# Kernel optimization log

Measured on AMD Instinct MI355X. Metric: run time of the kernel, lower is better.

## Reference

```python
import jax, jax.numpy as jnp
import numpy as np

N, E, F, H = 100000, 1600000, 128, 128


def setup_inputs() -> dict:
    key = jax.random.key(0)
    ks = jax.random.split(key, 32)
    def w(i, shape):
        fan_in = shape[0]
        return jax.random.normal(ks[i], shape, dtype=jnp.float32) / np.sqrt(fan_in)
    inp = {
        'x': jax.random.normal(ks[0], (N, F), dtype=jnp.float32),
        't': jax.random.randint(ks[1], (N,), 0, 2, dtype=jnp.int32),
        'z': jax.random.normal(ks[2], (N, H), dtype=jnp.float32),
        'edge_index': jax.random.randint(ks[3], (2, E), 0, N, dtype=jnp.int32),
        # GCNConv weights (PyG: out = scatter(norm * (xW)) + b)
        'W_o': w(4, (F, H)), 'b_o': jnp.zeros((H,), jnp.float32),
        'W_t': w(5, (F, H)), 'b_t': jnp.zeros((H,), jnp.float32),
        # masked attention: Linear(2H, 1)
        'a_w': w(6, (2 * H, 1)), 'a_b': jnp.zeros((1,), jnp.float32),
        # encoder_final: Linear(2H, H)
        'W_enc': w(7, (2 * H, H)), 'b_enc': jnp.zeros((H,), jnp.float32),
        # predictor heads (3 linears each)
        'p1_W1': w(8, (H, H)), 'p1_b1': jnp.zeros((H,), jnp.float32),
        'p1_W2': w(9, (H, H)), 'p1_b2': jnp.zeros((H,), jnp.float32),
        'p1_W3': w(10, (H, 1)), 'p1_b3': jnp.zeros((1,), jnp.float32),
        'p0_W1': w(11, (H, H)), 'p0_b1': jnp.zeros((H,), jnp.float32),
        'p0_W2': w(12, (H, H)), 'p0_b2': jnp.zeros((H,), jnp.float32),
        'p0_W3': w(13, (H, 1)), 'p0_b3': jnp.zeros((1,), jnp.float32),
        # discriminator head
        'd_W1': w(14, (H, H)), 'd_b1': jnp.zeros((H,), jnp.float32),
        'd_W2': w(15, (H, H)), 'd_b2': jnp.zeros((H,), jnp.float32),
        'd_W3': w(16, (H, 1)), 'd_b3': jnp.zeros((1,), jnp.float32),
    }
    return inp


def _mlp3(x, W1, b1, W2, b2, W3, b3):
    h = jax.nn.leaky_relu(x @ W1 + b1, 0.2)
    h = jax.nn.leaky_relu(h @ W2 + b2, 0.2)
    return h @ W3 + b3


def _gcn(x, W, b, src, dst, norm, n):
    xw = x @ W                                   # [N,H]
    agg = jax.ops.segment_sum(xw[src] * norm[:, None], dst, num_segments=n)
    return agg + b


def reference(x, t, z, edge_index, W_o, b_o, W_t, b_t, a_w, a_b, W_enc, b_enc,
              p1_W1, p1_b1, p1_W2, p1_b2, p1_W3, p1_b3,
              p0_W1, p0_b1, p0_W2, p0_b2, p0_W3, p0_b3,
              d_W1, d_b1, d_W2, d_b2, d_W3, d_b3):
    n = x.shape[0]
    src, dst = edge_index[0], edge_index[1]
    # --- GCN with self-loops and symmetric normalization ---
    loop = jnp.arange(n, dtype=src.dtype)
    src2 = jnp.concatenate([src, loop])
    dst2 = jnp.concatenate([dst, loop])
    deg = jax.ops.segment_sum(jnp.ones_like(dst2, jnp.float32), dst2, num_segments=n)
    dinv = jax.lax.rsqrt(deg)                    # deg >= 1 (self loops)
    norm = dinv[src2] * dinv[dst2]               # [E+N]
    r_o = jax.nn.relu(_gcn(x, W_o, b_o, src2, dst2, norm, n))
    r_t = jax.nn.relu(_gcn(x, W_t, b_t, src2, dst2, norm, n))
    cat = jnp.concatenate([r_o, r_t], axis=-1)   # [N,2H]
    # --- masked attention over edges: only treated sources attend ---
    e = (cat @ a_w + a_b)[:, 0]                  # [N]
    logits = jax.nn.leaky_relu(e[src] + e[dst], 0.2)   # [E]
    mask = (t[src] > 0).astype(jnp.float32)
    m = jax.ops.segment_max(logits, dst, num_segments=n)
    m = jnp.where(jnp.isfinite(m), m, 0.0)
    w = jnp.exp(logits - m[dst]) * mask
    denom = jax.ops.segment_sum(w, dst, num_segments=n) + 1e-16
    alpha = w / denom[dst]                       # [E]
    h = jax.ops.segment_sum(r_t[src] * alpha[:, None], dst, num_segments=n)  # [N,H]
    # --- heads ---
    z_enc = jnp.concatenate([r_o, h], axis=-1) @ W_enc + b_enc   # [N,H]
    pred_1 = _mlp3(z_enc, p1_W1, p1_b1, p1_W2, p1_b2, p1_W3, p1_b3)[:, 0]
    pred_0 = _mlp3(z_enc, p0_W1, p0_b1, p0_W2, p0_b2, p0_W3, p0_b3)[:, 0]
    pred = jnp.where(t > 0, pred_1, pred_0)[:, None]             # [N,1]
    pred_t = jax.nn.sigmoid(_mlp3(r_t, d_W1, d_b1, d_W2, d_b2, d_W3, d_b3))  # [N,1]
    return pred_t, pred, z_enc
```

## Files before the change

### kernel.cpp

```cpp
#include <hip/hip_runtime.h>
#include <hip/hip_bf16.h>
#include <math.h>


using bf16x8 = __attribute__((ext_vector_type(8))) short;
using s16x8  = __attribute__((ext_vector_type(8))) short;
using f32x4  = __attribute__((ext_vector_type(4))) float;

static __device__ __forceinline__ float lrelu02(float x) { return x > 0.f ? x : 0.2f * x; }

static __device__ __forceinline__ unsigned short f2bf(float f) {
    unsigned u = __float_as_uint(f);
    unsigned r = u + 0x7FFF + ((u >> 16) & 1);
    return (unsigned short)(r >> 16);
}
static __device__ __forceinline__ float bf2f(unsigned short h) {
    return __uint_as_float(((unsigned)h) << 16);
}
static __device__ __forceinline__ float bflo(unsigned u) { return __uint_as_float(u << 16); }
static __device__ __forceinline__ float bfhi(unsigned u) { return __uint_as_float(u & 0xFFFF0000u); }


__global__ void k_zero_i32(int* __restrict__ p, int n) {
    int i = blockIdx.x * blockDim.x + threadIdx.x;
    int stride = gridDim.x * blockDim.x;
    for (; i < n; i += stride) p[i] = 0;
}

__global__ void k_copy_i32(const int* __restrict__ a, int* __restrict__ b, int n) {
    int i = blockIdx.x * blockDim.x + threadIdx.x;
    if (i < n) b[i] = a[i];
}

__global__ __launch_bounds__(256) void k_bhist(const int* __restrict__ src,
                                               const int* __restrict__ dst,
                                               const int* __restrict__ t,
                                               int* __restrict__ bhist,
                                               int* __restrict__ bhist_m,
                                               int e, int shift) {
    __shared__ int h[256], hm[256];
    h[threadIdx.x] = 0; hm[threadIdx.x] = 0;
    __syncthreads();
    int i = blockIdx.x * blockDim.x + threadIdx.x;
    int stride = gridDim.x * blockDim.x;
    for (; i < e; i += stride) {
        int b = dst[i] >> shift;
        atomicAdd(&h[b], 1);
        if (t[src[i]] > 0) atomicAdd(&hm[b], 1);
    }
    __syncthreads();
    if (h[threadIdx.x]) atomicAdd(&bhist[threadIdx.x], h[threadIdx.x]);
    if (hm[threadIdx.x]) atomicAdd(&bhist_m[threadIdx.x], hm[threadIdx.x]);
}

__global__ __launch_bounds__(256) void k_scanb(const int* __restrict__ bsum,
                                               int* __restrict__ boff, int nb) {
    __shared__ int s[256];
    int t = threadIdx.x;
    int v = (t < nb) ? bsum[t] : 0;
    s[t] = v;
    __syncthreads();
    for (int off = 1; off < 256; off <<= 1) {
        int u = (t >= off) ? s[t - off] : 0;
        __syncthreads();
        s[t] += u;
        __syncthreads();
    }
    if (t < nb) boff[t] = s[t] - v;
    if (t == nb - 1) boff[nb] = s[t];
}

__global__ __launch_bounds__(256) void k_fillB(const int* __restrict__ src,
                                               const int* __restrict__ dst,
                                               const int* __restrict__ t,
                                               int* __restrict__ bcur,
                                               int* __restrict__ ebuf,
                                               int e, int shift) {
    __shared__ int h[256];
    const int EPT = 16;
    int blk_base = blockIdx.x * 256 * EPT;
    h[threadIdx.x] = 0;
    __syncthreads();
    int pk[EPT], bk[EPT];
#pragma unroll
    for (int j = 0; j < EPT; ++j) {
        int i = blk_base + threadIdx.x + j * 256;
        if (i < e) {
            int s = src[i], d = dst[i];
            int b = d >> shift;
            bk[j] = b;
            int tb = (t[s] > 0) ? 1 : 0;
            pk[j] = s | ((d - (b << shift)) << 20) | (tb << 29);
            atomicAdd(&h[b], 1);
        } else bk[j] = -1;
    }
    __syncthreads();
    int cnt = h[threadIdx.x];
    int base = 0;
    if (cnt > 0) base = atomicAdd(&bcur[threadIdx.x], cnt);
    __syncthreads();
    h[threadIdx.x] = base;
    __syncthreads();
#pragma unroll
    for (int j = 0; j < EPT; ++j) {
        if (bk[j] >= 0) {
            int pos = atomicAdd(&h[bk[j]], 1);
            ebuf[pos] = pk[j];
        }
    }
}

__global__ __launch_bounds__(256) void k_sortC(const int* __restrict__ ebuf,
                                               const int* __restrict__ bbase,
                                               const int* __restrict__ bbase_m,
                                               int* __restrict__ indptr,
                                               int* __restrict__ indptr_m,
                                               float* __restrict__ dinv,
                                               int* __restrict__ out_all,
                                               int* __restrict__ out_m,
                                               int n, int shift, int NB) {
    __shared__ int cnt[512], cnt_m[512];
    __shared__ int cur[512], cur_m[512];
    __shared__ int tmp[256];
    int tid = threadIdx.x;
    int b = blockIdx.x;
    int lo = bbase[b], hi = bbase[b + 1];
    int lom = bbase_m[b];
    int dbase = b << shift;
    for (int j = tid; j < 512; j += 256) { cnt[j] = 0; cnt_m[j] = 0; }
    __syncthreads();
    for (int i = lo + tid; i < hi; i += 256) {
        int pk = ebuf[i];
        int dlo = (pk >> 20) & 511;
        atomicAdd(&cnt[dlo], 1);
        if (pk >> 29) atomicAdd(&cnt_m[dlo], 1);
    }
    __syncthreads();
    int c0 = cnt[2 * tid], c1 = cnt[2 * tid + 1];
    int ps = c0 + c1;
    tmp[tid] = ps;
    __syncthreads();
    for (int off = 1; off < 256; off <<= 1) {
        int u = (tid >= off) ? tmp[tid - off] : 0;
        __syncthreads();
        tmp[tid] += u;
        __syncthreads();
    }
    int pre = tmp[tid] - ps;
    cur[2 * tid] = pre;
    cur[2 * tid + 1] = pre + c0;
    __syncthreads();
    int m0 = cnt_m[2 * tid], m1 = cnt_m[2 * tid + 1];
    int psm = m0 + m1;
    tmp[tid] = psm;
    __syncthreads();
    for (int off = 1; off < 256; off <<= 1) {
        int u = (tid >= off) ? tmp[tid - off] : 0;
        __syncthreads();
        tmp[tid] += u;
        __syncthreads();
    }
    int prem = tmp[tid] - psm;
    cur_m[2 * tid] = prem;
    cur_m[2 * tid + 1] = prem + m0;
    __syncthreads();
    int nd = n - dbase; if (nd > 512) nd = 512;
    for (int j = tid; j < nd; j += 256) {
        indptr[dbase + j] = lo + cur[j];
        indptr_m[dbase + j] = lom + cur_m[j];
        dinv[dbase + j] = rsqrtf((float)cnt[j] + 1.0f);
    }
    if (b == 0 && tid == 0) {
        indptr[n] = bbase[NB];
        indptr_m[n] = bbase_m[NB];
    }
    __syncthreads();
    for (int i = lo + tid; i < hi; i += 256) {
        int pk = ebuf[i];
        int s = pk & 0xFFFFF;
        int dlo = (pk >> 20) & 511;
        int pos = lo + atomicAdd(&cur[dlo], 1);
        out_all[pos] = s;
        if (pk >> 29) {
            int pm = lom + atomicAdd(&cur_m[dlo], 1);
            out_m[pm] = s;
        }
    }
}


__global__ void k_cvt_pre(const float* __restrict__ x, const float* __restrict__ dinv,
                          unsigned short* __restrict__ xp, int total4) {
    int i = blockIdx.x * blockDim.x + threadIdx.x;
    int stride = gridDim.x * blockDim.x;
    for (; i < total4; i += stride) {
        float dv = dinv[i >> 5];
        float4 v = ((const float4*)x)[i];
        ushort4 o;
        o.x = f2bf(v.x * dv); o.y = f2bf(v.y * dv);
        o.z = f2bf(v.z * dv); o.w = f2bf(v.w * dv);
        ((ushort4*)xp)[i] = o;
    }
}

__global__ void k_wt(const float* __restrict__ W, unsigned short* __restrict__ Wt,
                     int K, int Nc) {
    int i = blockIdx.x * blockDim.x + threadIdx.x;
    if (i >= K * Nc) return;
    int k = i / Nc, j = i % Nc;
    Wt[(size_t)j * K + k] = f2bf(W[i]);
}

__global__ void k_wcat_t(const float* __restrict__ Wo, const float* __restrict__ Wt_in,
                         unsigned short* __restrict__ Wt) {
    int i = blockIdx.x * blockDim.x + threadIdx.x;
    if (i >= 256 * 128) return;
    int j = i >> 7, k = i & 127;
    float v = (j < 128) ? Wo[(k << 7) + j] : Wt_in[(k << 7) + j - 128];
    Wt[i] = f2bf(v);
}

__global__ __launch_bounds__(256) void k_aggx(const unsigned short* __restrict__ xp,
                                              const int* __restrict__ indptr,
                                              const int* __restrict__ srcs,
                                              const float* __restrict__ dinv,
                                              unsigned short* __restrict__ aggx, int n) {
    int wv = threadIdx.x >> 6, lane = threadIdx.x & 63;
    int v = blockIdx.x * 4 + wv;
    if (v >= n) return;
    const unsigned* xp2 = (const unsigned*)xp;
    int beg = indptr[v], end = indptr[v + 1];
    unsigned sv = xp2[(size_t)v * 64 + lane];
    float a0 = bflo(sv), a1 = bfhi(sv);
    int i = beg;
    for (; i + 8 <= end; i += 8) {
        int s0 = srcs[i], s1 = srcs[i + 1], s2 = srcs[i + 2], s3 = srcs[i + 3];
        int s4 = srcs[i + 4], s5 = srcs[i + 5], s6 = srcs[i + 6], s7 = srcs[i + 7];
        unsigned u0 = xp2[(size_t)s0 * 64 + lane];
        unsigned u1 = xp2[(size_t)s1 * 64 + lane];
        unsigned u2 = xp2[(size_t)s2 * 64 + lane];
        unsigned u3 = xp2[(size_t)s3 * 64 + lane];
        unsigned u4 = xp2[(size_t)s4 * 64 + lane];
        unsigned u5 = xp2[(size_t)s5 * 64 + lane];
        unsigned u6 = xp2[(size_t)s6 * 64 + lane];
        unsigned u7 = xp2[(size_t)s7 * 64 + lane];
        a0 += bflo(u0) + bflo(u1) + bflo(u2) + bflo(u3)
            + bflo(u4) + bflo(u5) + bflo(u6) + bflo(u7);
        a1 += bfhi(u0) + bfhi(u1) + bfhi(u2) + bfhi(u3)
            + bfhi(u4) + bfhi(u5) + bfhi(u6) + bfhi(u7);
    }
    for (; i + 4 <= end; i += 4) {
        int s0 = srcs[i], s1 = srcs[i + 1], s2 = srcs[i + 2], s3 = srcs[i + 3];
        unsigned u0 = xp2[(size_t)s0 * 64 + lane];
        unsigned u1 = xp2[(size_t)s1 * 64 + lane];
        unsigned u2 = xp2[(size_t)s2 * 64 + lane];
        unsigned u3 = xp2[(size_t)s3 * 64 + lane];
        a0 += bflo(u0) + bflo(u1) + bflo(u2) + bflo(u3);
        a1 += bfhi(u0) + bfhi(u1) + bfhi(u2) + bfhi(u3);
    }
    for (; i < end; ++i) {
        unsigned u = xp2[(size_t)srcs[i] * 64 + lane];
        a0 += bflo(u); a1 += bfhi(u);
    }
    float dv = dinv[v];
    a0 *= dv; a1 *= dv;
    unsigned o = (unsigned)f2bf(a0) | ((unsigned)f2bf(a1) << 16);
    ((unsigned*)aggx)[(size_t)v * 64 + lane] = o;
}

__global__ __launch_bounds__(256) void k_gcn(const unsigned short* __restrict__ aggx,
                                             const unsigned short* __restrict__ Wcat,
                                             const float* __restrict__ b_o,
                                             const float* __restrict__ b_t,
                                             const float* __restrict__ a_w,
                                             const float* __restrict__ a_b,
                                             unsigned short* __restrict__ cat2,
                                             unsigned short* __restrict__ rt,
                                             float* __restrict__ e, int M) {
    __shared__ short ct[64][264];
    int wave = threadIdx.x >> 6, lane = threadIdx.x & 63;
    int row_base = blockIdx.x * 64 + wave * 16;
    int rA = row_base + (lane & 15);
    if (rA >= M) rA = M - 1;
    int koff = (lane >> 4) << 3;
    int colL = lane & 15;

    bf16x8 a[4];
#pragma unroll
    for (int ks = 0; ks < 4; ++ks)
        a[ks] = *(const bf16x8*)((const short*)aggx + (size_t)rA * 128 + (ks << 5) + koff);

    f32x4 acc[16];
#pragma unroll
    for (int cf = 0; cf < 16; ++cf) acc[cf] = (f32x4){0.f, 0.f, 0.f, 0.f};
#pragma unroll
    for (int ks = 0; ks < 4; ++ks)
#pragma unroll
        for (int cf = 0; cf < 16; ++cf) {
            bf16x8 b = *(const bf16x8*)((const short*)Wcat + (size_t)((cf << 4) + colL) * 128 + (ks << 5) + koff);
            acc[cf] = __builtin_amdgcn_mfma_f32_16x16x32_bf16(a[ks], b, acc[cf], 0, 0, 0);
        }

    float ep0 = 0.f, ep1 = 0.f, ep2 = 0.f, ep3 = 0.f;
    int rl0 = wave * 16 + ((lane >> 4) << 2);
#pragma unroll
    for (int cf = 0; cf < 16; ++cf) {
        int col = (cf << 4) + colL;
        float bv = (col < 128) ? b_o[col] : b_t[col - 128];
        float aw = a_w[col];
#pragma unroll
        for (int j = 0; j < 4; ++j) {
            float v = fmaxf(acc[cf][j] + bv, 0.f);
            if (j == 0) ep0 += v * aw;
            else if (j == 1) ep1 += v * aw;
            else if (j == 2) ep2 += v * aw;
            else ep3 += v * aw;
            ct[rl0 + j][col] = (short)f2bf(v);
        }
    }
#pragma unroll
    for (int mk = 1; mk < 16; mk <<= 1) {
        ep0 += __shfl_xor(ep0, mk); ep1 += __shfl_xor(ep1, mk);
        ep2 += __shfl_xor(ep2, mk); ep3 += __shfl_xor(ep3, mk);
    }
    if (colL == 0) {
        float ab = a_b[0];
        int r0 = row_base + ((lane >> 4) << 2);
        if (r0 + 0 < M) e[r0 + 0] = ep0 + ab;
        if (r0 + 1 < M) e[r0 + 1] = ep1 + ab;
        if (r0 + 2 < M) e[r0 + 2] = ep2 + ab;
        if (r0 + 3 < M) e[r0 + 3] = ep3 + ab;
    }
    __syncthreads();
    int base64 = blockIdx.x * 64;
    short* cp = (short*)cat2 + (size_t)base64 * 256;
    for (int j = threadIdx.x; j < 1024; j += 256) {
        int row = j >> 4;
        if (base64 + row < M)
            *(s16x8*)(cp + (size_t)row * 256 + ((j & 15) << 3)) =
                *(const s16x8*)&ct[row][(j & 15) << 3];
    }
    short* rp = (short*)rt + (size_t)base64 * 128;
    for (int j = threadIdx.x; j < 1024; j += 256) {
        int row = j >> 4;
        if (base64 + row < M)
            *(s16x8*)(rp + (size_t)row * 128 + ((j & 15) << 3)) =
                *(const s16x8*)&ct[row][128 + ((j & 15) << 3)];
    }
}

__global__ __launch_bounds__(256) void k_attn(const unsigned short* __restrict__ rt,
                                              const int* __restrict__ indptr_m,
                                              const int* __restrict__ srcs_m,
                                              const float* __restrict__ e,
                                              unsigned short* __restrict__ cat2, int n) {
    int wv = threadIdx.x >> 6, lane = threadIdx.x & 63;
    int v = blockIdx.x * 4 + wv;
    if (v >= n) return;
    float ev = e[v];
    int bm = indptr_m[v], em = indptr_m[v + 1];
    float m = -INFINITY;
    for (int i = bm + lane; i < em; i += 64)
        m = fmaxf(m, lrelu02(ev + e[srcs_m[i]]));
    for (int off = 32; off; off >>= 1) m = fmaxf(m, __shfl_xor(m, off));
    if (bm == em) m = 0.f;
    float h0 = 0.f, h1 = 0.f, wsum = 0.f;
    const unsigned* rt2 = (const unsigned*)rt;
    int i = bm;
    for (; i + 8 <= em; i += 8) {
        int s0 = srcs_m[i], s1 = srcs_m[i + 1], s2 = srcs_m[i + 2], s3 = srcs_m[i + 3];
        int s4 = srcs_m[i + 4], s5 = srcs_m[i + 5], s6 = srcs_m[i + 6], s7 = srcs_m[i + 7];
        float w0 = __expf(lrelu02(ev + e[s0]) - m);
        float w1 = __expf(lrelu02(ev + e[s1]) - m);
        float w2 = __expf(lrelu02(ev + e[s2]) - m);
        float w3 = __expf(lrelu02(ev + e[s3]) - m);
        float w4 = __expf(lrelu02(ev + e[s4]) - m);
        float w5 = __expf(lrelu02(ev + e[s5]) - m);
        float w6 = __expf(lrelu02(ev + e[s6]) - m);
        float w7 = __expf(lrelu02(ev + e[s7]) - m);
        unsigned u0 = rt2[(size_t)s0 * 64 + lane];
        unsigned u1 = rt2[(size_t)s1 * 64 + lane];
        unsigned u2 = rt2[(size_t)s2 * 64 + lane];
        unsigned u3 = rt2[(size_t)s3 * 64 + lane];
        unsigned u4 = rt2[(size_t)s4 * 64 + lane];
        unsigned u5 = rt2[(size_t)s5 * 64 + lane];
        unsigned u6 = rt2[(size_t)s6 * 64 + lane];
        unsigned u7 = rt2[(size_t)s7 * 64 + lane];
        wsum += w0 + w1 + w2 + w3 + w4 + w5 + w6 + w7;
        h0 += w0 * bflo(u0) + w1 * bflo(u1) + w2 * bflo(u2) + w3 * bflo(u3)
            + w4 * bflo(u4) + w5 * bflo(u5) + w6 * bflo(u6) + w7 * bflo(u7);
        h1 += w0 * bfhi(u0) + w1 * bfhi(u1) + w2 * bfhi(u2) + w3 * bfhi(u3)
            + w4 * bfhi(u4) + w5 * bfhi(u5) + w6 * bfhi(u6) + w7 * bfhi(u7);
    }
    for (; i < em; ++i) {
        int s = srcs_m[i];
        float w = __expf(lrelu02(ev + e[s]) - m);
        unsigned u = rt2[(size_t)s * 64 + lane];
        wsum += w;
        h0 += w * bflo(u);
        h1 += w * bfhi(u);
    }
    float inv = 1.f / (wsum + 1e-16f);
    unsigned o = (unsigned)f2bf(h0 * inv) | ((unsigned)f2bf(h1 * inv) << 16);
    ((unsigned*)(cat2 + (size_t)v * 256 + 128))[lane] = o;
}

__global__ __launch_bounds__(256) void k_tail(
    const unsigned short* __restrict__ cat2, const unsigned short* __restrict__ rt_bf,
    const unsigned short* __restrict__ Wenc, const float* __restrict__ b_enc,
    const unsigned short* __restrict__ W11, const float* __restrict__ b11,
    const unsigned short* __restrict__ W12, const float* __restrict__ b12,
    const float* __restrict__ W13, const float* __restrict__ b13,
    const unsigned short* __restrict__ W01, const float* __restrict__ b01,
    const unsigned short* __restrict__ W02, const float* __restrict__ b02,
    const float* __restrict__ W03, const float* __restrict__ b03,
    const unsigned short* __restrict__ Wd1, const float* __restrict__ bd1,
    const unsigned short* __restrict__ Wd2, const float* __restrict__ bd2,
    const float* __restrict__ Wd3, const float* __restrict__ bd3,
    const int* __restrict__ t, float* __restrict__ zenc,
    float* __restrict__ out, int M) {
    __shared__ __align__(16) char pool[128 * 136 * 2 + 64 * 136 * 2];
    short* Wa = (short*)pool;
    short* hb = (short*)(pool + 128 * 136 * 2);
    float* zt = (float*)pool;

    int wave = threadIdx.x >> 6, lane = threadIdx.x & 63;
    int row_base = blockIdx.x * 64 + wave * 16;
    int rA = row_base + (lane & 15);
    if (rA >= M) rA = M - 1;
    int koff = (lane >> 4) << 3;
    int colL = lane & 15;
    int base64 = blockIdx.x * 64;

    bf16x8 ra[4];
#pragma unroll
    for (int ks = 0; ks < 4; ++ks)
        ra[ks] = *(const bf16x8*)((const short*)rt_bf + (size_t)rA * 128 + (ks << 5) + koff);

    {
        const short* Ap = (const short*)cat2 + (size_t)rA * 256 + koff;
        const short* Bp = (const short*)Wenc + (size_t)colL * 256 + koff;
        f32x4 acc[8];
#pragma unroll
        for (int cf = 0; cf < 8; ++cf) acc[cf] = (f32x4){0.f, 0.f, 0.f, 0.f};
#pragma unroll
        for (int ks = 0; ks < 8; ++ks) {
            bf16x8 a = *(const bf16x8*)(Ap + (ks << 5));
#pragma unroll
            for (int cf = 0; cf < 8; ++cf) {
                bf16x8 b = *(const bf16x8*)(Bp + (size_t)(cf << 4) * 256 + (ks << 5));
                acc[cf] = __builtin_amdgcn_mfma_f32_16x16x32_bf16(a, b, acc[cf], 0, 0, 0);
            }
        }
        int rl0 = wave * 16 + ((lane >> 4) << 2);
#pragma unroll
        for (int cf = 0; cf < 8; ++cf) {
            int col = (cf << 4) + colL;
            float bv = b_enc[col];
#pragma unroll
            for (int j = 0; j < 4; ++j)
                zt[(rl0 + j) * 132 + col] = acc[cf][j] + bv;
        }
    }
    __syncthreads();
    {
        float* zp = zenc + (size_t)base64 * 128;
        for (int j = threadIdx.x; j < 2048; j += 256) {
            int row = j >> 5;
            if (base64 + row < M)
                *(float4*)(zp + (size_t)j * 4) = *(const float4*)&zt[row * 132 + ((j & 31) << 2)];
        }
    }
    bf16x8 za[4];
    {
        int rAl = wave * 16 + (lane & 15);
#pragma unroll
        for (int ks = 0; ks < 4; ++ks) {
            float4 v0 = *(const float4*)&zt[rAl * 132 + (ks << 5) + koff];
            float4 v1 = *(const float4*)&zt[rAl * 132 + (ks << 5) + koff + 4];
            za[ks][0] = (short)f2bf(v0.x); za[ks][1] = (short)f2bf(v0.y);
            za[ks][2] = (short)f2bf(v0.z); za[ks][3] = (short)f2bf(v0.w);
            za[ks][4] = (short)f2bf(v1.x); za[ks][5] = (short)f2bf(v1.y);
            za[ks][6] = (short)f2bf(v1.z); za[ks][7] = (short)f2bf(v1.w);
        }
    }

    float sp1[4], sp0[4], sdd[4];

    auto stage = [&](const unsigned short* W) {
        for (int i = threadIdx.x; i < 2048; i += 256) {
            int r = i >> 4, c = (i & 15) << 3;
            bf16x8 v = *(const bf16x8*)((const short*)W + (r << 7) + c);
            *(bf16x8*)(Wa + r * 136 + c) = v;
        }
    };

    auto run_head = [&](const bf16x8* A0,
                        const unsigned short* W1, const float* b1,
                        const unsigned short* W2, const float* b2,
                        const float* W3, const float* b3, float* sout) {
        __syncthreads();
        stage(W1);
        __syncthreads();
        f32x4 acc[8];
#pragma unroll
        for (int cf = 0; cf < 8; ++cf) acc[cf] = (f32x4){0.f, 0.f, 0.f, 0.f};
#pragma unroll
        for (int ks = 0; ks < 4; ++ks)
#pragma unroll
            for (int cf = 0; cf < 8; ++cf) {
                bf16x8 b = *(const bf16x8*)(Wa + ((cf << 4) + colL) * 136 + (ks << 5) + koff);
                acc[cf] = __builtin_amdgcn_mfma_f32_16x16x32_bf16(A0[ks], b, acc[cf], 0, 0, 0);
            }
        short* hw = hb + wave * 2176;
#pragma unroll
        for (int cf = 0; cf < 8; ++cf) {
            int col = (cf << 4) + colL;
            float bv = b1[col];
#pragma unroll
            for (int j = 0; j < 4; ++j)
                hw[(((lane >> 4) << 2) + j) * 136 + col] = (short)f2bf(lrelu02(acc[cf][j] + bv));
        }
        __syncthreads();
        stage(W2);
        __syncthreads();
        bf16x8 h1f[4];
#pragma unroll
        for (int ks = 0; ks < 4; ++ks)
            h1f[ks] = *(const bf16x8*)(hw + colL * 136 + (ks << 5) + koff);
#pragma unroll
        for (int cf = 0; cf < 8; ++cf) acc[cf] = (f32x4){0.f, 0.f, 0.f, 0.f};
#pragma unroll
        for (int ks = 0; ks < 4; ++ks)
#pragma unroll
            for (int cf = 0; cf < 8; ++cf) {
                bf16x8 b = *(const bf16x8*)(Wa + ((cf << 4) + colL) * 136 + (ks << 5) + koff);
                acc[cf] = __builtin_amdgcn_mfma_f32_16x16x32_bf16(h1f[ks], b, acc[cf], 0, 0, 0);
            }
        float s0 = 0.f, s1 = 0.f, s2 = 0.f, s3 = 0.f;
#pragma unroll
        for (int cf = 0; cf < 8; ++cf) {
            int col = (cf << 4) + colL;
            float w3 = W3[col], bv = b2[col];
            s0 += lrelu02(acc[cf][0] + bv) * w3;
            s1 += lrelu02(acc[cf][1] + bv) * w3;
            s2 += lrelu02(acc[cf][2] + bv) * w3;
            s3 += lrelu02(acc[cf][3] + bv) * w3;
        }
#pragma unroll
        for (int mk = 1; mk < 16; mk <<= 1) {
            s0 += __shfl_xor(s0, mk); s1 += __shfl_xor(s1, mk);
            s2 += __shfl_xor(s2, mk); s3 += __shfl_xor(s3, mk);
        }
        float bb = b3[0];
        sout[0] = s0 + bb; sout[1] = s1 + bb; sout[2] = s2 + bb; sout[3] = s3 + bb;
    };

    run_head(za, W11, b11, W12, b12, W13, b13, sp1);
    run_head(za, W01, b01, W02, b02, W03, b03, sp0);
    run_head(ra, Wd1, bd1, Wd2, bd2, Wd3, bd3, sdd);

    if (colL == 0) {
#pragma unroll
        for (int j = 0; j < 4; ++j) {
            int row = row_base + ((lane >> 4) << 2) + j;
            if (row < M) {
                out[row] = 1.f / (1.f + __expf(-sdd[j]));
                out[M + row] = (t[row] > 0) ? sp1[j] : sp0[j];
            }
        }
    }
}


extern "C" void kernel_launch(void* const* d_in, const int* in_sizes, int n_in,
                              void* d_out, int out_size, void* d_ws, size_t ws_size,
                              hipStream_t stream) {
    const float* x     = (const float*)d_in[0];
    const int*   t     = (const int*)d_in[1];
    const int*   ei    = (const int*)d_in[3];
    const float* W_o   = (const float*)d_in[4];
    const float* b_o   = (const float*)d_in[5];
    const float* W_t   = (const float*)d_in[6];
    const float* b_t   = (const float*)d_in[7];
    const float* a_w   = (const float*)d_in[8];
    const float* a_b   = (const float*)d_in[9];
    const float* W_enc = (const float*)d_in[10];
    const float* b_enc = (const float*)d_in[11];
    const float* p1_W1 = (const float*)d_in[12]; const float* p1_b1 = (const float*)d_in[13];
    const float* p1_W2 = (const float*)d_in[14]; const float* p1_b2 = (const float*)d_in[15];
    const float* p1_W3 = (const float*)d_in[16]; const float* p1_b3 = (const float*)d_in[17];
    const float* p0_W1 = (const float*)d_in[18]; const float* p0_b1 = (const float*)d_in[19];
    const float* p0_W2 = (const float*)d_in[20]; const float* p0_b2 = (const float*)d_in[21];
    const float* p0_W3 = (const float*)d_in[22]; const float* p0_b3 = (const float*)d_in[23];
    const float* d_W1  = (const float*)d_in[24]; const float* d_b1  = (const float*)d_in[25];
    const float* d_W2  = (const float*)d_in[26]; const float* d_b2  = (const float*)d_in[27];
    const float* d_W3  = (const float*)d_in[28]; const float* d_b3  = (const float*)d_in[29];

    const int n = in_sizes[1];
    const int E = in_sizes[3] / 2;
    const int* src = ei;
    const int* dst = ei + E;

    float* out  = (float*)d_out;
    float* zenc = out + 2 * (size_t)n;

    const int shift = 9;
    const int NB = (n + (1 << shift) - 1) >> shift;

    char* base = (char*)d_ws;
    size_t o = 0;
    auto alloc = [&](size_t bytes) { char* p = base + o; o += (bytes + 255) & ~(size_t)255; return p; };
    unsigned short* xp_bf   = (unsigned short*)alloc((size_t)n * 128 * 2);
    unsigned short* aggx_bf = (unsigned short*)alloc((size_t)n * 128 * 2);
    unsigned short* cat2_bf = (unsigned short*)alloc((size_t)n * 256 * 2);
    unsigned short* rt_bf   = (unsigned short*)alloc((size_t)n * 128 * 2);
    float* dinv = (float*)alloc((size_t)n * 4);
    float* evec = (float*)alloc((size_t)n * 4);
    unsigned short* Wcat_t = (unsigned short*)alloc(256 * 128 * 2);
    unsigned short* Wenc_t = (unsigned short*)alloc(128 * 256 * 2);
    unsigned short* Wp1a_t = (unsigned short*)alloc(128 * 128 * 2);
    unsigned short* Wp1b_t = (unsigned short*)alloc(128 * 128 * 2);
    unsigned short* Wp0a_t = (unsigned short*)alloc(128 * 128 * 2);
    unsigned short* Wp0b_t = (unsigned short*)alloc(128 * 128 * 2);
    unsigned short* Wda_t  = (unsigned short*)alloc(128 * 128 * 2);
    unsigned short* Wdb_t  = (unsigned short*)alloc(128 * 128 * 2);
    int* indptr     = (int*)alloc(((size_t)n + 1) * 4);
    int* indptr_m   = (int*)alloc(((size_t)n + 1) * 4);
    int* bhist      = (int*)alloc(257 * 4);
    int* bhist_m    = (int*)alloc(257 * 4);
    int* bbase      = (int*)alloc(257 * 4);
    int* bbase_m    = (int*)alloc(257 * 4);
    int* bcur       = (int*)alloc(257 * 4);
    int* src_sorted = (int*)alloc((size_t)E * 4);
    int* src_mask   = (int*)alloc((size_t)E * 4);
    int* ebuf       = (int*)alloc((size_t)E * 4);

    const int mt = (n + 63) / 64;

    k_zero_i32<<<1, 256, 0, stream>>>(bhist, 257);
    k_zero_i32<<<1, 256, 0, stream>>>(bhist_m, 257);
    k_bhist<<<1024, 256, 0, stream>>>(src, dst, t, bhist, bhist_m, E, shift);
    k_scanb<<<1, 256, 0, stream>>>(bhist, bbase, NB);
    k_scanb<<<1, 256, 0, stream>>>(bhist_m, bbase_m, NB);
    k_copy_i32<<<1, 256, 0, stream>>>(bbase, bcur, NB);
    k_fillB<<<(E + 4095) / 4096, 256, 0, stream>>>(src, dst, t, bcur, ebuf, E, shift);
    k_sortC<<<NB, 256, 0, stream>>>(ebuf, bbase, bbase_m, indptr, indptr_m, dinv,
                                    src_sorted, src_mask, n, shift, NB);

    k_cvt_pre<<<2048, 256, 0, stream>>>(x, dinv, xp_bf, n * 32);
    k_wcat_t<<<128, 256, 0, stream>>>(W_o, W_t, Wcat_t);
    k_wt<<<128, 256, 0, stream>>>(W_enc, Wenc_t, 256, 128);
    k_wt<<<64, 256, 0, stream>>>(p1_W1, Wp1a_t, 128, 128);
    k_wt<<<64, 256, 0, stream>>>(p1_W2, Wp1b_t, 128, 128);
    k_wt<<<64, 256, 0, stream>>>(p0_W1, Wp0a_t, 128, 128);
    k_wt<<<64, 256, 0, stream>>>(p0_W2, Wp0b_t, 128, 128);
    k_wt<<<64, 256, 0, stream>>>(d_W1, Wda_t, 128, 128);
    k_wt<<<64, 256, 0, stream>>>(d_W2, Wdb_t, 128, 128);

    k_aggx<<<(n + 3) / 4, 256, 0, stream>>>(xp_bf, indptr, src_sorted, dinv, aggx_bf, n);

    k_gcn<<<mt, 256, 0, stream>>>(aggx_bf, Wcat_t, b_o, b_t, a_w, a_b,
                                  cat2_bf, rt_bf, evec, n);

    k_attn<<<(n + 3) / 4, 256, 0, stream>>>(rt_bf, indptr_m, src_mask, evec, cat2_bf, n);

    k_tail<<<mt, 256, 0, stream>>>(cat2_bf, rt_bf, Wenc_t, b_enc,
                                   Wp1a_t, p1_b1, Wp1b_t, p1_b2, p1_W3, p1_b3,
                                   Wp0a_t, p0_b1, Wp0b_t, p0_b2, p0_W3, p0_b3,
                                   Wda_t, d_b1, Wdb_t, d_b2, d_W3, d_b3,
                                   t, zenc, out, n);
}
```

Measured before the change: 443.6 us.

## Process 128 rows per tail block and merge small setup kernels

```diff
diff --git a/kernel.cpp b/kernel.cpp
--- a/kernel.cpp
+++ b/kernel.cpp
@@ -25,11 +25,6 @@
     int i = blockIdx.x * blockDim.x + threadIdx.x;
     int stride = gridDim.x * blockDim.x;
     for (; i < n; i += stride) p[i] = 0;
-}
-
-__global__ void k_copy_i32(const int* __restrict__ a, int* __restrict__ b, int n) {
-    int i = blockIdx.x * blockDim.x + threadIdx.x;
-    if (i < n) b[i] = a[i];
 }
 
 __global__ __launch_bounds__(256) void k_bhist(const int* __restrict__ src,
@@ -53,11 +48,14 @@
     if (hm[threadIdx.x]) atomicAdd(&bhist_m[threadIdx.x], hm[threadIdx.x]);
 }
 
-__global__ __launch_bounds__(256) void k_scanb(const int* __restrict__ bsum,
-                                               int* __restrict__ boff, int nb) {
+__global__ __launch_bounds__(256) void k_scan2(const int* __restrict__ bhist,
+                                               const int* __restrict__ bhist_m,
+                                               int* __restrict__ bbase,
+                                               int* __restrict__ bbase_m,
+                                               int* __restrict__ bcur, int nb) {
     __shared__ int s[256];
     int t = threadIdx.x;
-    int v = (t < nb) ? bsum[t] : 0;
+    int v = (t < nb) ? bhist[t] : 0;
     s[t] = v;
     __syncthreads();
     for (int off = 1; off < 256; off <<= 1) {
@@ -66,8 +64,20 @@
         s[t] += u;
         __syncthreads();
     }
-    if (t < nb) boff[t] = s[t] - v;
-    if (t == nb - 1) boff[nb] = s[t];
+    if (t < nb) { bbase[t] = s[t] - v; bcur[t] = s[t] - v; }
+    if (t == nb - 1) bbase[nb] = s[t];
+    __syncthreads();
+    int v2 = (t < nb) ? bhist_m[t] : 0;
+    s[t] = v2;
+    __syncthreads();
+    for (int off = 1; off < 256; off <<= 1) {
+        int u = (t >= off) ? s[t - off] : 0;
+        __syncthreads();
+        s[t] += u;
+        __syncthreads();
+    }
+    if (t < nb) bbase_m[t] = s[t] - v2;
+    if (t == nb - 1) bbase_m[nb] = s[t];
 }
 
 __global__ __launch_bounds__(256) void k_fillB(const int* __restrict__ src,
@@ -203,21 +213,39 @@
     }
 }
 
-__global__ void k_wt(const float* __restrict__ W, unsigned short* __restrict__ Wt,
-                     int K, int Nc) {
-    int i = blockIdx.x * blockDim.x + threadIdx.x;
-    if (i >= K * Nc) return;
-    int k = i / Nc, j = i % Nc;
-    Wt[(size_t)j * K + k] = f2bf(W[i]);
-}
-
-__global__ void k_wcat_t(const float* __restrict__ Wo, const float* __restrict__ Wt_in,
-                         unsigned short* __restrict__ Wt) {
-    int i = blockIdx.x * blockDim.x + threadIdx.x;
-    if (i >= 256 * 128) return;
-    int j = i >> 7, k = i & 127;
-    float v = (j < 128) ? Wo[(k << 7) + j] : Wt_in[(k << 7) + j - 128];
-    Wt[i] = f2bf(v);
+__global__ void k_wprep(const float* __restrict__ Wo, const float* __restrict__ Wti,
+                        const float* __restrict__ Wenc,
+                        const float* __restrict__ p1W1, const float* __restrict__ p1W2,
+                        const float* __restrict__ p0W1, const float* __restrict__ p0W2,
+                        const float* __restrict__ dW1, const float* __restrict__ dW2,
+                        unsigned short* __restrict__ Wcat_t,
+                        unsigned short* __restrict__ Wenc_t,
+                        unsigned short* __restrict__ o1, unsigned short* __restrict__ o2,
+                        unsigned short* __restrict__ o3, unsigned short* __restrict__ o4,
+                        unsigned short* __restrict__ o5, unsigned short* __restrict__ o6) {
+    int idx = blockIdx.x * 256 + threadIdx.x;
+    if (idx < 32768) {
+        int j = idx >> 7, k = idx & 127;
+        float v = (j < 128) ? Wo[(k << 7) + j] : Wti[(k << 7) + j - 128];
+        Wcat_t[idx] = f2bf(v);
+    } else if (idx < 65536) {
+        int i = idx - 32768;
+        Wenc_t[(size_t)(i & 127) * 256 + (i >> 7)] = f2bf(Wenc[i]);
+    } else {
+        int i2 = idx - 65536;
+        int h = i2 >> 14;
+        int i = i2 & 16383;
+        const float* W; unsigned short* O;
+        switch (h) {
+            case 0: W = p1W1; O = o1; break;
+            case 1: W = p1W2; O = o2; break;
+            case 2: W = p0W1; O = o3; break;
+            case 3: W = p0W2; O = o4; break;
+            case 4: W = dW1;  O = o5; break;
+            default: W = dW2; O = o6; break;
+        }
+        O[(i & 127) * 128 + (i >> 7)] = f2bf(W[i]);
+    }
 }
 
 __global__ __launch_bounds__(256) void k_aggx(const unsigned short* __restrict__ xp,
@@ -419,26 +447,29 @@
     const float* __restrict__ Wd3, const float* __restrict__ bd3,
     const int* __restrict__ t, float* __restrict__ zenc,
     float* __restrict__ out, int M) {
-    __shared__ __align__(16) char pool[128 * 136 * 2 + 64 * 136 * 2];
+    const int WS = 132;
+    const int ZS = 133;
+    __shared__ __align__(16) char pool[64 * 133 * 4 + 64 * 132 * 2];
     short* Wa = (short*)pool;
-    short* hb = (short*)(pool + 128 * 136 * 2);
     float* zt = (float*)pool;
+    short* hb = (short*)(pool + 64 * 133 * 4);
 
     int wave = threadIdx.x >> 6, lane = threadIdx.x & 63;
-    int row_base = blockIdx.x * 64 + wave * 16;
-    int rA = row_base + (lane & 15);
-    if (rA >= M) rA = M - 1;
+    int colL = lane & 15;
     int koff = (lane >> 4) << 3;
-    int colL = lane & 15;
-    int base64 = blockIdx.x * 64;
-
-    bf16x8 ra[4];
-#pragma unroll
-    for (int ks = 0; ks < 4; ++ks)
-        ra[ks] = *(const bf16x8*)((const short*)rt_bf + (size_t)rA * 128 + (ks << 5) + koff);
-
-    {
-        const short* Ap = (const short*)cat2 + (size_t)rA * 256 + koff;
+    int base128 = blockIdx.x * 128;
+
+    int rAc[2];
+#pragma unroll
+    for (int c = 0; c < 2; ++c) {
+        int rA = base128 + c * 64 + wave * 16 + colL;
+        rAc[c] = (rA >= M) ? M - 1 : rA;
+    }
+
+    bf16x8 za[2][4];
+#pragma unroll
+    for (int c = 0; c < 2; ++c) {
+        const short* Ap = (const short*)cat2 + (size_t)rAc[c] * 256 + koff;
         const short* Bp = (const short*)Wenc + (size_t)colL * 256 + koff;
         f32x4 acc[8];
 #pragma unroll
@@ -459,116 +490,133 @@
             float bv = b_enc[col];
 #pragma unroll
             for (int j = 0; j < 4; ++j)
-                zt[(rl0 + j) * 132 + col] = acc[cf][j] + bv;
-        }
-    }
-    __syncthreads();
-    {
-        float* zp = zenc + (size_t)base64 * 128;
-        for (int j = threadIdx.x; j < 2048; j += 256) {
-            int row = j >> 5;
-            if (base64 + row < M)
-                *(float4*)(zp + (size_t)j * 4) = *(const float4*)&zt[row * 132 + ((j & 31) << 2)];
-        }
-    }
-    bf16x8 za[4];
-    {
-        int rAl = wave * 16 + (lane & 15);
-#pragma unroll
-        for (int ks = 0; ks < 4; ++ks) {
-            float4 v0 = *(const float4*)&zt[rAl * 132 + (ks << 5) + koff];
-            float4 v1 = *(const float4*)&zt[rAl * 132 + (ks << 5) + koff + 4];
-            za[ks][0] = (short)f2bf(v0.x); za[ks][1] = (short)f2bf(v0.y);
-            za[ks][2] = (short)f2bf(v0.z); za[ks][3] = (short)f2bf(v0.w);
-            za[ks][4] = (short)f2bf(v1.x); za[ks][5] = (short)f2bf(v1.y);
-            za[ks][6] = (short)f2bf(v1.z); za[ks][7] = (short)f2bf(v1.w);
-        }
-    }
-
-    float sp1[4], sp0[4], sdd[4];
+                zt[(rl0 + j) * ZS + col] = acc[cf][j] + bv;
+        }
+        __syncthreads();
+        {
+            float* zp = zenc + (size_t)(base128 + c * 64) * 128;
+            for (int j = threadIdx.x; j < 2048; j += 256) {
+                int row = j >> 5;
+                if (base128 + c * 64 + row < M)
+                    *(float4*)(zp + (size_t)j * 4) = *(const float4*)&zt[row * ZS + ((j & 31) << 2)];
+            }
+        }
+        {
+            int rAl = wave * 16 + colL;
+#pragma unroll
+            for (int ks = 0; ks < 4; ++ks) {
+                float4 v0 = *(const float4*)&zt[rAl * ZS + (ks << 5) + koff];
+                float4 v1 = *(const float4*)&zt[rAl * ZS + (ks << 5) + koff + 4];
+                za[c][ks][0] = (short)f2bf(v0.x); za[c][ks][1] = (short)f2bf(v0.y);
+                za[c][ks][2] = (short)f2bf(v0.z); za[c][ks][3] = (short)f2bf(v0.w);
+                za[c][ks][4] = (short)f2bf(v1.x); za[c][ks][5] = (short)f2bf(v1.y);
+                za[c][ks][6] = (short)f2bf(v1.z); za[c][ks][7] = (short)f2bf(v1.w);
+            }
+        }
+        __syncthreads();
+    }
+
+    float sp1[2][4], sp0[2][4], sdd[2][4];
 
     auto stage = [&](const unsigned short* W) {
         for (int i = threadIdx.x; i < 2048; i += 256) {
             int r = i >> 4, c = (i & 15) << 3;
             bf16x8 v = *(const bf16x8*)((const short*)W + (r << 7) + c);
-            *(bf16x8*)(Wa + r * 136 + c) = v;
+            *(bf16x8*)(Wa + r * WS + c) = v;
         }
     };
 
-    auto run_head = [&](const bf16x8* A0,
+    auto run_head = [&](const bf16x8 (*A0)[4],
                         const unsigned short* W1, const float* b1,
                         const unsigned short* W2, const float* b2,
-                        const float* W3, const float* b3, float* sout) {
-        __syncthreads();
+                        const float* W3, const float* b3, float (*sout)[4]) {
         stage(W1);
         __syncthreads();
-        f32x4 acc[8];
-#pragma unroll
-        for (int cf = 0; cf < 8; ++cf) acc[cf] = (f32x4){0.f, 0.f, 0.f, 0.f};
-#pragma unroll
-        for (int ks = 0; ks < 4; ++ks)
+        bf16x8 h1f[2][4];
+        short* hw = hb + wave * 16 * WS;
+#pragma unroll
+        for (int c = 0; c < 2; ++c) {
+            f32x4 acc[8];
+#pragma unroll
+            for (int cf = 0; cf < 8; ++cf) acc[cf] = (f32x4){0.f, 0.f, 0.f, 0.f};
+#pragma unroll
+            for (int ks = 0; ks < 4; ++ks)
+#pragma unroll
+                for (int cf = 0; cf < 8; ++cf) {
+                    bf16x8 b = *(const bf16x8*)(Wa + ((cf << 4) + colL) * WS + (ks << 5) + koff);
+                    acc[cf] = __builtin_amdgcn_mfma_f32_16x16x32_bf16(A0[c][ks], b, acc[cf], 0, 0, 0);
+                }
 #pragma unroll
             for (int cf = 0; cf < 8; ++cf) {
-                bf16x8 b = *(const bf16x8*)(Wa + ((cf << 4) + colL) * 136 + (ks << 5) + koff);
-                acc[cf] = __builtin_amdgcn_mfma_f32_16x16x32_bf16(A0[ks], b, acc[cf], 0, 0, 0);
+                int col = (cf << 4) + colL;
+                float bv = b1[col];
+#pragma unroll
+                for (int j = 0; j < 4; ++j)
+                    hw[(((lane >> 4) << 2) + j) * WS + col] = (short)f2bf(lrelu02(acc[cf][j] + bv));
             }
-        short* hw = hb + wave * 2176;
-#pragma unroll
-        for (int cf = 0; cf < 8; ++cf) {
-            int col = (cf << 4) + colL;
-            float bv = b1[col];
-#pragma unroll
-            for (int j = 0; j < 4; ++j)
-                hw[(((lane >> 4) << 2) + j) * 136 + col] = (short)f2bf(lrelu02(acc[cf][j] + bv));
+#pragma unroll
+            for (int ks = 0; ks < 4; ++ks)
+                h1f[c][ks] = *(const bf16x8*)(hw + colL * WS + (ks << 5) + koff);
         }
         __syncthreads();
         stage(W2);
         __syncthreads();
-        bf16x8 h1f[4];
-#pragma unroll
-        for (int ks = 0; ks < 4; ++ks)
-            h1f[ks] = *(const bf16x8*)(hw + colL * 136 + (ks << 5) + koff);
-#pragma unroll
-        for (int cf = 0; cf < 8; ++cf) acc[cf] = (f32x4){0.f, 0.f, 0.f, 0.f};
-#pragma unroll
-        for (int ks = 0; ks < 4; ++ks)
+#pragma unroll
+        for (int c = 0; c < 2; ++c) {
+            f32x4 acc[8];
+#pragma unroll
+            for (int cf = 0; cf < 8; ++cf) acc[cf] = (f32x4){0.f, 0.f, 0.f, 0.f};
+#pragma unroll
+            for (int ks = 0; ks < 4; ++ks)
+#pragma unroll
+                for (int cf = 0; cf < 8; ++cf) {
+                    bf16x8 b = *(const bf16x8*)(Wa + ((cf << 4) + colL) * WS + (ks << 5) + koff);
+                    acc[cf] = __builtin_amdgcn_mfma_f32_16x16x32_bf16(h1f[c][ks], b, acc[cf], 0, 0, 0);
+                }
+            float s0 = 0.f, s1 = 0.f, s2 = 0.f, s3 = 0.f;
 #pragma unroll
             for (int cf = 0; cf < 8; ++cf) {
-                bf16x8 b = *(const bf16x8*)(Wa + ((cf << 4) + colL) * 136 + (ks << 5) + koff);
-                acc[cf] = __builtin_amdgcn_mfma_f32_16x16x32_bf16(h1f[ks], b, acc[cf], 0, 0, 0);
+                int col = (cf << 4) + colL;
+                float w3 = W3[col], bv = b2[col];
+                s0 += lrelu02(acc[cf][0] + bv) * w3;
+                s1 += lrelu02(acc[cf][1] + bv) * w3;
+                s2 += lrelu02(acc[cf][2] + bv) * w3;
+                s3 += lrelu02(acc[cf][3] + bv) * w3;
             }
-        float s0 = 0.f, s1 = 0.f, s2 = 0.f, s3 = 0.f;
-#pragma unroll
-        for (int cf = 0; cf < 8; ++cf) {
-            int col = (cf << 4) + colL;
-            float w3 = W3[col], bv = b2[col];
-            s0 += lrelu02(acc[cf][0] + bv) * w3;
-            s1 += lrelu02(acc[cf][1] + bv) * w3;
-            s2 += lrelu02(acc[cf][2] + bv) * w3;
-            s3 += lrelu02(acc[cf][3] + bv) * w3;
-        }
-#pragma unroll
-        for (int mk = 1; mk < 16; mk <<= 1) {
-            s0 += __shfl_xor(s0, mk); s1 += __shfl_xor(s1, mk);
-            s2 += __shfl_xor(s2, mk); s3 += __shfl_xor(s3, mk);
-        }
-        float bb = b3[0];
-        sout[0] = s0 + bb; sout[1] = s1 + bb; sout[2] = s2 + bb; sout[3] = s3 + bb;
+#pragma unroll
+            for (int mk = 1; mk < 16; mk <<= 1) {
+                s0 += __shfl_xor(s0, mk); s1 += __shfl_xor(s1, mk);
+                s2 += __shfl_xor(s2, mk); s3 += __shfl_xor(s3, mk);
+            }
+            float bb = b3[0];
+            sout[c][0] = s0 + bb; sout[c][1] = s1 + bb;
+            sout[c][2] = s2 + bb; sout[c][3] = s3 + bb;
+        }
+        __syncthreads();
     };
 
     run_head(za, W11, b11, W12, b12, W13, b13, sp1);
     run_head(za, W01, b01, W02, b02, W03, b03, sp0);
+
+    bf16x8 ra[2][4];
+#pragma unroll
+    for (int c = 0; c < 2; ++c)
+#pragma unroll
+        for (int ks = 0; ks < 4; ++ks)
+            ra[c][ks] = *(const bf16x8*)((const short*)rt_bf + (size_t)rAc[c] * 128 + (ks << 5) + koff);
     run_head(ra, Wd1, bd1, Wd2, bd2, Wd3, bd3, sdd);
 
     if (colL == 0) {
 #pragma unroll
-        for (int j = 0; j < 4; ++j) {
-            int row = row_base + ((lane >> 4) << 2) + j;
-            if (row < M) {
-                out[row] = 1.f / (1.f + __expf(-sdd[j]));
-                out[M + row] = (t[row] > 0) ? sp1[j] : sp0[j];
+        for (int c = 0; c < 2; ++c)
+#pragma unroll
+            for (int j = 0; j < 4; ++j) {
+                int row = base128 + c * 64 + wave * 16 + ((lane >> 4) << 2) + j;
+                if (row < M) {
+                    out[row] = 1.f / (1.f + __expf(-sdd[c][j]));
+                    out[M + row] = (t[row] > 0) ? sp1[c][j] : sp0[c][j];
+                }
             }
-        }
     }
 }
 
@@ -627,8 +675,8 @@
     unsigned short* Wdb_t  = (unsigned short*)alloc(128 * 128 * 2);
     int* indptr     = (int*)alloc(((size_t)n + 1) * 4);
     int* indptr_m   = (int*)alloc(((size_t)n + 1) * 4);
-    int* bhist      = (int*)alloc(257 * 4);
-    int* bhist_m    = (int*)alloc(257 * 4);
+    int* bhist      = (int*)alloc(514 * 4);
+    int* bhist_m    = bhist + 257;
     int* bbase      = (int*)alloc(257 * 4);
     int* bbase_m    = (int*)alloc(257 * 4);
     int* bcur       = (int*)alloc(257 * 4);
@@ -636,27 +684,20 @@
     int* src_mask   = (int*)alloc((size_t)E * 4);
     int* ebuf       = (int*)alloc((size_t)E * 4);
 
-    const int mt = (n + 63) / 64;
-
-    k_zero_i32<<<1, 256, 0, stream>>>(bhist, 257);
-    k_zero_i32<<<1, 256, 0, stream>>>(bhist_m, 257);
+    const int mt  = (n + 63) / 64;
+    const int mt2 = (n + 127) / 128;
+
+    k_zero_i32<<<1, 256, 0, stream>>>(bhist, 514);
     k_bhist<<<1024, 256, 0, stream>>>(src, dst, t, bhist, bhist_m, E, shift);
-    k_scanb<<<1, 256, 0, stream>>>(bhist, bbase, NB);
-    k_scanb<<<1, 256, 0, stream>>>(bhist_m, bbase_m, NB);
-    k_copy_i32<<<1, 256, 0, stream>>>(bbase, bcur, NB);
+    k_scan2<<<1, 256, 0, stream>>>(bhist, bhist_m, bbase, bbase_m, bcur, NB);
     k_fillB<<<(E + 4095) / 4096, 256, 0, stream>>>(src, dst, t, bcur, ebuf, E, shift);
     k_sortC<<<NB, 256, 0, stream>>>(ebuf, bbase, bbase_m, indptr, indptr_m, dinv,
                                     src_sorted, src_mask, n, shift, NB);
 
+    k_wprep<<<640, 256, 0, stream>>>(W_o, W_t, W_enc, p1_W1, p1_W2, p0_W1, p0_W2,
+                                     d_W1, d_W2, Wcat_t, Wenc_t,
+                                     Wp1a_t, Wp1b_t, Wp0a_t, Wp0b_t, Wda_t, Wdb_t);
     k_cvt_pre<<<2048, 256, 0, stream>>>(x, dinv, xp_bf, n * 32);
-    k_wcat_t<<<128, 256, 0, stream>>>(W_o, W_t, Wcat_t);
-    k_wt<<<128, 256, 0, stream>>>(W_enc, Wenc_t, 256, 128);
-    k_wt<<<64, 256, 0, stream>>>(p1_W1, Wp1a_t, 128, 128);
-    k_wt<<<64, 256, 0, stream>>>(p1_W2, Wp1b_t, 128, 128);
-    k_wt<<<64, 256, 0, stream>>>(p0_W1, Wp0a_t, 128, 128);
-    k_wt<<<64, 256, 0, stream>>>(p0_W2, Wp0b_t, 128, 128);
-    k_wt<<<64, 256, 0, stream>>>(d_W1, Wda_t, 128, 128);
-    k_wt<<<64, 256, 0, stream>>>(d_W2, Wdb_t, 128, 128);
 
     k_aggx<<<(n + 3) / 4, 256, 0, stream>>>(xp_bf, indptr, src_sorted, dinv, aggx_bf, n);
 
@@ -665,9 +706,9 @@
 
     k_attn<<<(n + 3) / 4, 256, 0, stream>>>(rt_bf, indptr_m, src_mask, evec, cat2_bf, n);
 
-    k_tail<<<mt, 256, 0, stream>>>(cat2_bf, rt_bf, Wenc_t, b_enc,
-                                   Wp1a_t, p1_b1, Wp1b_t, p1_b2, p1_W3, p1_b3,
-                                   Wp0a_t, p0_b1, Wp0b_t, p0_b2, p0_W3, p0_b3,
-                                   Wda_t, d_b1, Wdb_t, d_b2, d_W3, d_b3,
-                                   t, zenc, out, n);
-}
+    k_tail<<<mt2, 256, 0, stream>>>(cat2_bf, rt_bf, Wenc_t, b_enc,
+                                    Wp1a_t, p1_b1, Wp1b_t, p1_b2, p1_W3, p1_b3,
+                                    Wp0a_t, p0_b1, Wp0b_t, p0_b2, p0_W3, p0_b3,
+                                    Wda_t, d_b1, Wdb_t, d_b2, d_W3, d_b3,
+                                    t, zenc, out, n);
+}
```

New measurement: 551.9 us. 1.24x slower.
